# Kernel tuning notes

Hardware: AMD Instinct MI355X
Metric: run time of the kernel (lower is better)

Reference implementation:

```python
import jax, jax.numpy as jnp
import numpy as np

B, T, D, H, C = 128, 256, 256, 1024, 1000

def _xavier(k, shape):
    std = (2.0 / (shape[0] + shape[1])) ** 0.5
    return jax.random.normal(k, shape, dtype=jnp.float32) * std

def setup_inputs() -> dict:
    key = jax.random.key(0)
    ks = jax.random.split(key, 10)
    inp = {"x": jax.random.normal(ks[0], (B, T, D), dtype=jnp.float32)}
    for n, k in zip(["W_gx", "W_ix", "W_fx", "W_ox"], ks[1:5]):
        inp[n] = _xavier(k, (D, H))
    for n, k in zip(["W_gh", "W_ih", "W_fh", "W_oh"], ks[5:9]):
        inp[n] = _xavier(k, (H, H))
    inp["W_ph"] = _xavier(ks[9], (H, C))
    for n in ["b_g", "b_i", "b_f", "b_o"]:
        inp[n] = jnp.zeros((H,), dtype=jnp.float32)
    inp["b_p"] = jnp.zeros((C,), dtype=jnp.float32)
    return inp

def reference(x, W_gx, W_ix, W_fx, W_ox, W_gh, W_ih, W_fh, W_oh, W_ph,
              b_g, b_i, b_f, b_o, b_p):
    b, t, d = x.shape
    h_dim = W_gh.shape[0]
    # Precompute all input projections in batched GEMMs: [T, B, H]
    xg = jnp.einsum('btd,dh->tbh', x, W_gx) + b_g
    xi = jnp.einsum('btd,dh->tbh', x, W_ix) + b_i
    xf = jnp.einsum('btd,dh->tbh', x, W_fx) + b_f
    xo = jnp.einsum('btd,dh->tbh', x, W_ox) + b_o

    def step(carry, xs):
        h, c = carry
        pg, pi, pf, po = xs
        g = jnp.tanh(pg + h @ W_gh)
        i = jax.nn.sigmoid(pi + h @ W_ih)
        f = jax.nn.sigmoid(pf + h @ W_fh)
        o = jax.nn.sigmoid(po + h @ W_oh)
        c = g * i + c * f
        h = jnp.tanh(c) * o
        return (h, c), None

    h0 = jnp.zeros((b, h_dim), dtype=x.dtype)
    c0 = jnp.zeros((b, h_dim), dtype=x.dtype)
    (h_T, _), _ = jax.lax.scan(step, (h0, c0), (xg, xi, xf, xo))
    p = h_T @ W_ph + b_p  # [B, num_classes]
    return jax.nn.log_softmax(p, axis=1)
```

## Files before the change

### kernel.cpp

```cpp
#include <hip/hip_runtime.h>
#include <hip/hip_bf16.h>

#define B_ 128
#define T_ 256
#define D_ 256
#define H_ 1024
#define C_ 1000

typedef __attribute__((ext_vector_type(8))) short short8;
typedef __attribute__((ext_vector_type(4))) float floatx4;

static __device__ __forceinline__ unsigned short f2bf(float f) {
  unsigned int u = __builtin_bit_cast(unsigned int, f);
  u += 0x7fffu + ((u >> 16) & 1u);
  return (unsigned short)(u >> 16);
}
static __device__ __forceinline__ float bf2f(unsigned short s) {
  unsigned int u = ((unsigned int)s) << 16;
  return __builtin_bit_cast(float, u);
}
static __device__ __forceinline__ float sigm(float z) {
  return 1.0f / (1.0f + __expf(-z));
}
static __device__ __forceinline__ float tanh_fast(float z) {
  z = fminf(fmaxf(z, -15.f), 15.f);
  float e = __expf(2.f * z);
  return (e - 1.f) / (e + 1.f);
}

__global__ __launch_bounds__(256) void pack_all(
    const float* __restrict__ Wgx, const float* __restrict__ Wix,
    const float* __restrict__ Wfx, const float* __restrict__ Wox,
    const float* __restrict__ Wgh, const float* __restrict__ Wih,
    const float* __restrict__ Wfh, const float* __restrict__ Woh,
    unsigned short* __restrict__ Wp,
    const float* __restrict__ x, unsigned short* __restrict__ xb) {
  int blk = blockIdx.x;
  if (blk < 2560) {
    int t = blk * 256 + threadIdx.x;
    int L = t & 63;
    int g = (t >> 6) & 3;
    int rest = t >> 8;
    int kc = rest % 40;
    int jb = rest / 40;
    int n = L & 15, q = L >> 4;
    int j = jb * 16 + n;
    const float* Wh = (g == 0) ? Wgh : (g == 1) ? Wih : (g == 2) ? Wfh : Woh;
    const float* Wx = (g == 0) ? Wgx : (g == 1) ? Wix : (g == 2) ? Wfx : Wox;
    int k0 = kc * 32 + q * 8;
    unsigned int w[4];
#pragma unroll
    for (int i = 0; i < 4; i++) {
      int ka = k0 + 2 * i, kb = k0 + 2 * i + 1;
      float fa = (ka < H_) ? Wh[(size_t)ka * H_ + j] : Wx[(size_t)(ka - H_) * H_ + j];
      float fb = (kb < H_) ? Wh[(size_t)kb * H_ + j] : Wx[(size_t)(kb - H_) * H_ + j];
      w[i] = (unsigned int)f2bf(fa) | ((unsigned int)f2bf(fb) << 16);
    }
    uint4 v = {w[0], w[1], w[2], w[3]};
    *((uint4*)(Wp + (size_t)t * 8)) = v;
  } else {
    int idx = (blk - 2560) * 256 + threadIdx.x;
    int d8 = idx & 31;
    int tt = (idx >> 5) & 255;
    int b = idx >> 13;
    const float* src = x + ((size_t)b * T_ + tt) * D_ + d8 * 8;
    int rt = b >> 4, kcx = d8 >> 2, q = d8 & 3, m = b & 15;
    size_t dst = ((((size_t)tt * 8 + rt) * 8 + kcx) * 64 + (q * 16 + m)) * 8;
    unsigned int w[4];
#pragma unroll
    for (int i = 0; i < 4; i++) {
      float fa = src[2 * i], fb = src[2 * i + 1];
      w[i] = (unsigned int)f2bf(fa) | ((unsigned int)f2bf(fb) << 16);
    }
    uint4 v = {w[0], w[1], w[2], w[3]};
    *((uint4*)(xb + dst)) = v;
  }
}

__global__ __launch_bounds__(256, 1) void lstm_all(
    unsigned short* __restrict__ hb0, unsigned short* __restrict__ hb1,
    const unsigned short* __restrict__ Wp, const unsigned short* __restrict__ xb,
    const float* __restrict__ bg, const float* __restrict__ bi,
    const float* __restrict__ bf_, const float* __restrict__ bo,
    unsigned int* __restrict__ fl) {
  __shared__ unsigned short WL[32 * 4 * 64 * 8];
  __shared__ float xg[2][4][32][17];
  __shared__ float bb[4][16];

  const int tid = threadIdx.x;
  const int bid = blockIdx.x;
  const int jb = bid >> 2, rtq = bid & 3;
  const int w = tid >> 6, lane = tid & 63;
  const int rt01 = w & 1, kh = w >> 1;
  const int rt = rtq * 2 + rt01;
  const int grp = rtq * 64;

  {
    const uint4* src = (const uint4*)(Wp + (size_t)jb * (40 * 4 * 64 * 8));
    uint4* dst = (uint4*)WL;
#pragma unroll
    for (int i = 0; i < 32; i++) dst[i * 256 + tid] = src[i * 256 + tid];
  }
  if (tid < 64) {
    int g = tid >> 4, n = tid & 15;
    const float* bs = (g == 0) ? bg : (g == 1) ? bi : (g == 2) ? bf_ : bo;
    bb[g][n] = bs[jb * 16 + n];
  }
  {
    int rr = tid >> 3, n0 = (tid & 7) * 2;
    int r = rtq * 32 + rr;
    int rt_r = r >> 4, m = r & 15;
    int j = jb * 16 + n0;
    size_t dst = ((size_t)(rt_r * 32 + (j >> 5)) * 64 + (((j >> 3) & 3) * 16 + m)) * 8 + (j & 7);
    __hip_atomic_store((unsigned int*)(hb0 + dst), 0u, __ATOMIC_RELAXED,
                       __HIP_MEMORY_SCOPE_AGENT);
  }
  float c0 = 0.f, c1 = 0.f;

  const short8* BpX = (const short8*)Wp + (size_t)jb * (40 * 4 * 64) + lane;
  const short8* BL = (const short8*)WL + (size_t)kh * 4096 + lane;
  const int kc0 = kh * 16;
  const int kx0 = kh * 4;

  short8 bxw[4][4];
#pragma unroll
  for (int i = 0; i < 4; i++)
#pragma unroll
    for (int g = 0; g < 4; g++)
      bxw[i][g] = BpX[(size_t)((32 + kx0 + i) * 4 + g) * 64];

  __syncthreads();

  if (tid == 0)
    __hip_atomic_store(&fl[grp + jb], 1u, __ATOMIC_RELAXED, __HIP_MEMORY_SCOPE_AGENT);

  floatx4 xa0 = {0.f, 0.f, 0.f, 0.f};
  floatx4 xa1 = xa0, xa2 = xa0, xa3 = xa0;
  {
    const short8* Ax = (const short8*)xb + (((size_t)0 * 8 + rt) * 8 + kx0) * 64 + lane;
    short8 ax[4];
#pragma unroll
    for (int i = 0; i < 4; i++) ax[i] = Ax[(size_t)i * 64];
#pragma unroll
    for (int i = 0; i < 4; i++) {
      xa0 = __builtin_amdgcn_mfma_f32_16x16x32_bf16(ax[i], bxw[i][0], xa0, 0, 0, 0);
      xa1 = __builtin_amdgcn_mfma_f32_16x16x32_bf16(ax[i], bxw[i][1], xa1, 0, 0, 0);
      xa2 = __builtin_amdgcn_mfma_f32_16x16x32_bf16(ax[i], bxw[i][2], xa2, 0, 0, 0);
      xa3 = __builtin_amdgcn_mfma_f32_16x16x32_bf16(ax[i], bxw[i][3], xa3, 0, 0, 0);
    }
  }

  if (w == 0) {
    while (true) {
      unsigned int v = __hip_atomic_load(&fl[grp + lane], __ATOMIC_RELAXED,
                                         __HIP_MEMORY_SCOPE_AGENT);
      if (__all((int)(v >= 1u))) break;
    }
  }
  __syncthreads();
  asm volatile("" ::: "memory");

#pragma unroll 1
  for (int t = 0; t < 256; t++) {
    const unsigned short* hc = (t & 1) ? hb1 : hb0;
    unsigned short* hn = (t & 1) ? hb0 : hb1;

    const unsigned short* Ahp = hc + ((size_t)(rt * 32 + kc0) * 64 + lane) * 8;
    unsigned long long hq[32];
#pragma unroll
    for (int i = 0; i < 16; i++) {
      hq[2 * i] = __hip_atomic_load((const unsigned long long*)(Ahp + (size_t)i * 512),
                                    __ATOMIC_RELAXED, __HIP_MEMORY_SCOPE_AGENT);
      hq[2 * i + 1] = __hip_atomic_load((const unsigned long long*)(Ahp + (size_t)i * 512 + 4),
                                        __ATOMIC_RELAXED, __HIP_MEMORY_SCOPE_AGENT);
    }
    int tn = (t < 255) ? t + 1 : 255;
    const short8* Axn = (const short8*)xb + (((size_t)tn * 8 + rt) * 8 + kx0) * 64 + lane;
    short8 ax[4];
#pragma unroll
    for (int i = 0; i < 4; i++) ax[i] = Axn[(size_t)i * 64];

    floatx4 a0 = xa0, a1 = xa1, a2 = xa2, a3 = xa3;
#pragma unroll
    for (int kc = 0; kc < 16; kc++) {
      union { unsigned long long q[2]; short8 v; } u;
      u.q[0] = hq[2 * kc];
      u.q[1] = hq[2 * kc + 1];
      short8 av = u.v;
      short8 b0 = BL[(size_t)(kc * 4 + 0) * 64];
      short8 b1v = BL[(size_t)(kc * 4 + 1) * 64];
      short8 b2 = BL[(size_t)(kc * 4 + 2) * 64];
      short8 b3 = BL[(size_t)(kc * 4 + 3) * 64];
      a0 = __builtin_amdgcn_mfma_f32_16x16x32_bf16(av, b0, a0, 0, 0, 0);
      a1 = __builtin_amdgcn_mfma_f32_16x16x32_bf16(av, b1v, a1, 0, 0, 0);
      a2 = __builtin_amdgcn_mfma_f32_16x16x32_bf16(av, b2, a2, 0, 0, 0);
      a3 = __builtin_amdgcn_mfma_f32_16x16x32_bf16(av, b3, a3, 0, 0, 0);
    }

    {
      int cl = lane & 15, q = lane >> 4;
#pragma unroll
      for (int p = 0; p < 4; p++) {
        int rrow = rt01 * 16 + q * 4 + p;
        xg[kh][0][rrow][cl] = a0[p];
        xg[kh][1][rrow][cl] = a1[p];
        xg[kh][2][rrow][cl] = a2[p];
        xg[kh][3][rrow][cl] = a3[p];
      }
    }
    __syncthreads();

    {
      int rr = tid >> 3, n0 = (tid & 7) * 2;
      int r = rtq * 32 + rr;
      int rt_r = r >> 4, m = r & 15;
      unsigned int packed = 0;
#pragma unroll
      for (int u = 0; u < 2; u++) {
        int n = n0 + u;
        float pg = xg[0][0][rr][n] + xg[1][0][rr][n] + bb[0][n];
        float pi_ = xg[0][1][rr][n] + xg[1][1][rr][n] + bb[1][n];
        float pf = xg[0][2][rr][n] + xg[1][2][rr][n] + bb[2][n];
        float po = xg[0][3][rr][n] + xg[1][3][rr][n] + bb[3][n];
        float gg = tanh_fast(pg);
        float ii = sigm(pi_);
        float ff = sigm(pf);
        float oo = sigm(po);
        float cold = u ? c1 : c0;
        float cn = gg * ii + cold * ff;
        if (u) c1 = cn; else c0 = cn;
        float hv = tanh_fast(cn) * oo;
        packed |= ((unsigned int)f2bf(hv)) << (16 * u);
      }
      int j = jb * 16 + n0;
      size_t dst = ((size_t)(rt_r * 32 + (j >> 5)) * 64 + (((j >> 3) & 3) * 16 + m)) * 8 + (j & 7);
      __hip_atomic_store((unsigned int*)(hn + dst), packed, __ATOMIC_RELAXED,
                         __HIP_MEMORY_SCOPE_AGENT);
    }
    __syncthreads();

    if (tid == 0)
      __hip_atomic_store(&fl[grp + jb], (unsigned int)t + 2u, __ATOMIC_RELAXED,
                         __HIP_MEMORY_SCOPE_AGENT);

    xa0 = (floatx4){0.f, 0.f, 0.f, 0.f};
    xa1 = xa0; xa2 = xa0; xa3 = xa0;
#pragma unroll
    for (int i = 0; i < 4; i++) {
      xa0 = __builtin_amdgcn_mfma_f32_16x16x32_bf16(ax[i], bxw[i][0], xa0, 0, 0, 0);
      xa1 = __builtin_amdgcn_mfma_f32_16x16x32_bf16(ax[i], bxw[i][1], xa1, 0, 0, 0);
      xa2 = __builtin_amdgcn_mfma_f32_16x16x32_bf16(ax[i], bxw[i][2], xa2, 0, 0, 0);
      xa3 = __builtin_amdgcn_mfma_f32_16x16x32_bf16(ax[i], bxw[i][3], xa3, 0, 0, 0);
    }

    if (w == 0) {
      unsigned int tgt = (unsigned int)t + 2u;
      while (true) {
        unsigned int v = __hip_atomic_load(&fl[grp + lane], __ATOMIC_RELAXED,
                                           __HIP_MEMORY_SCOPE_AGENT);
        if (__all((int)(v >= tgt))) break;
      }
    }
    __syncthreads();
    asm volatile("" ::: "memory");
  }
}

__global__ __launch_bounds__(256) void proj_mfma(const unsigned short* __restrict__ hB,
                                                 const float* __restrict__ Wph,
                                                 const float* __restrict__ bp,
                                                 float* __restrict__ Lbuf) {
  __shared__ float pacc[4][16][17];
  const int tid = threadIdx.x;
  const int rt = blockIdx.x & 7;
  const int cb = blockIdx.x >> 3;
  const int w = tid >> 6, lane = tid & 63;
  const int n = lane & 15, q = lane >> 4;
  const int j = cb * 16 + n;
  const bool jv = (j < C_);

  floatx4 acc = {0.f, 0.f, 0.f, 0.f};
  const short8* Ah = (const short8*)hB + ((size_t)rt * 32) * 64 + lane;
#pragma unroll
  for (int kq = 0; kq < 8; kq++) {
    int kc = w * 8 + kq;
    short8 a = Ah[(size_t)kc * 64];
    int k0 = kc * 32 + q * 8;
    unsigned int wb[4];
#pragma unroll
    for (int i = 0; i < 4; i++) {
      float fa = jv ? Wph[(size_t)(k0 + 2 * i) * C_ + j] : 0.f;
      float fb = jv ? Wph[(size_t)(k0 + 2 * i + 1) * C_ + j] : 0.f;
      wb[i] = (unsigned int)f2bf(fa) | ((unsigned int)f2bf(fb) << 16);
    }
    union { unsigned int u[4]; short8 v; } bu;
    bu.u[0] = wb[0]; bu.u[1] = wb[1]; bu.u[2] = wb[2]; bu.u[3] = wb[3];
    acc = __builtin_amdgcn_mfma_f32_16x16x32_bf16(a, bu.v, acc, 0, 0, 0);
  }
#pragma unroll
  for (int p = 0; p < 4; p++) pacc[w][q * 4 + p][n] = acc[p];
  __syncthreads();

  {
    int r = tid >> 4, nn = tid & 15;
    int jj = cb * 16 + nn;
    float s = pacc[0][r][nn] + pacc[1][r][nn] + pacc[2][r][nn] + pacc[3][r][nn];
    s += (jj < C_) ? bp[jj] : 0.f;
    Lbuf[(size_t)(rt * 16 + r) * 1008 + jj] = s;
  }
}

__global__ __launch_bounds__(256) void softmax_k(const float* __restrict__ Lbuf,
                                                 float* __restrict__ out) {
  __shared__ float red[256];
  int row = blockIdx.x, tid = threadIdx.x;
  const float* Lr = Lbuf + (size_t)row * 1008;
  bool v3 = (tid + 768 < C_);
  float a0 = Lr[tid];
  float a1 = Lr[tid + 256];
  float a2 = Lr[tid + 512];
  float a3 = v3 ? Lr[tid + 768] : 0.f;

  float mx = fmaxf(fmaxf(a0, a1), a2);
  if (v3) mx = fmaxf(mx, a3);
  red[tid] = mx;
  __syncthreads();
  for (int s = 128; s > 0; s >>= 1) {
    if (tid < s) red[tid] = fmaxf(red[tid], red[tid + s]);
    __syncthreads();
  }
  float M = red[0];
  __syncthreads();
  float se = __expf(a0 - M) + __expf(a1 - M) + __expf(a2 - M);
  if (v3) se += __expf(a3 - M);
  red[tid] = se;
  __syncthreads();
  for (int s = 128; s > 0; s >>= 1) {
    if (tid < s) red[tid] += red[tid + s];
    __syncthreads();
  }
  float lse = M + logf(red[0]);
  out[(size_t)row * C_ + tid] = a0 - lse;
  out[(size_t)row * C_ + tid + 256] = a1 - lse;
  out[(size_t)row * C_ + tid + 512] = a2 - lse;
  if (v3) out[(size_t)row * C_ + tid + 768] = a3 - lse;
}

extern "C" void kernel_launch(void* const* d_in, const int* in_sizes, int n_in,
                              void* d_out, int out_size, void* d_ws, size_t ws_size,
                              hipStream_t stream) {
  const float* x   = (const float*)d_in[0];
  const float* Wgx = (const float*)d_in[1];
  const float* Wix = (const float*)d_in[2];
  const float* Wfx = (const float*)d_in[3];
  const float* Wox = (const float*)d_in[4];
  const float* Wgh = (const float*)d_in[5];
  const float* Wih = (const float*)d_in[6];
  const float* Wfh = (const float*)d_in[7];
  const float* Woh = (const float*)d_in[8];
  const float* Wph = (const float*)d_in[9];
  const float* bg  = (const float*)d_in[10];
  const float* bi  = (const float*)d_in[11];
  const float* bf  = (const float*)d_in[12];
  const float* bo  = (const float*)d_in[13];
  const float* bp  = (const float*)d_in[14];

  char* ws = (char*)d_ws;
  unsigned short* Wp = (unsigned short*)ws;
  size_t off = 10485760;
  unsigned short* xb = (unsigned short*)(ws + off);
  float* Lbuf = (float*)xb;
  off += 16777216;
  unsigned short* h0 = (unsigned short*)(ws + off); off += 262144;
  unsigned short* h1 = (unsigned short*)(ws + off); off += 262144;
  unsigned int* fl = (unsigned int*)(ws + off); off += 4096;

  hipMemsetAsync(fl, 0, 4096, stream);

  pack_all<<<6656, 256, 0, stream>>>(Wgx, Wix, Wfx, Wox, Wgh, Wih, Wfh, Woh, Wp, x, xb);

  void* args[] = {(void*)&h0, (void*)&h1, (void*)&Wp, (void*)&xb,
                  (void*)&bg, (void*)&bi, (void*)&bf, (void*)&bo, (void*)&fl};
  hipError_t cerr = hipLaunchCooperativeKernel((void*)lstm_all, dim3(256), dim3(256),
                                               args, 0, stream);
  if (cerr != hipSuccess) {
    lstm_all<<<256, 256, 0, stream>>>(h0, h1, Wp, xb, bg, bi, bf, bo, fl);
  }

  proj_mfma<<<504, 256, 0, stream>>>(h0, Wph, bp, Lbuf);
  softmax_k<<<128, 256, 0, stream>>>(Lbuf, (float*)d_out);
}
```

Baseline: 1.122 ms.

## Use per-step h ring buffer, split weights between registers and LDS, per-wave polling

Replaces the double-buffered hidden state with a ring of 257 buffers, one per timestep, when the workspace is large enough. Each step then reads a fresh address with plain vector loads instead of agent-scope atomic loads. Half of the recurrent weight tiles (gates g,i) now stay in registers and only gates f,o stay in LDS. Every wave polls the flags for its own half of the group instead of wave 0 polling followed by a block barrier, and the last step skips the final sync. The risks are much higher register pressure, a large workspace footprint, and a reliance on caches not serving stale lines at new addresses.

```diff
diff --git a/kernel.cpp b/kernel.cpp
--- a/kernel.cpp
+++ b/kernel.cpp
@@ -82,8 +82,8 @@
     const unsigned short* __restrict__ Wp, const unsigned short* __restrict__ xb,
     const float* __restrict__ bg, const float* __restrict__ bi,
     const float* __restrict__ bf_, const float* __restrict__ bo,
-    unsigned int* __restrict__ fl) {
-  __shared__ unsigned short WL[32 * 4 * 64 * 8];
+    unsigned int* __restrict__ fl, int ring) {
+  __shared__ unsigned short WL[32 * 2 * 64 * 8];
   __shared__ float xg[2][4][32][17];
   __shared__ float bb[4][16];
 
@@ -95,11 +95,17 @@
   const int rt = rtq * 2 + rt01;
   const int grp = rtq * 64;
 
+  (void)__hip_atomic_load(&fl[0], __ATOMIC_ACQUIRE, __HIP_MEMORY_SCOPE_AGENT);
+
   {
-    const uint4* src = (const uint4*)(Wp + (size_t)jb * (40 * 4 * 64 * 8));
-    uint4* dst = (uint4*)WL;
-#pragma unroll
-    for (int i = 0; i < 32; i++) dst[i * 256 + tid] = src[i * 256 + tid];
+    const uint4* srcW = (const uint4*)Wp + (size_t)jb * (40 * 4 * 64);
+    uint4* dstW = (uint4*)WL;
+#pragma unroll
+    for (int it = 0; it < 16; it++) {
+      int d = it * 256 + tid;
+      int kc = d >> 7, r = d & 127;
+      dstW[d] = srcW[(size_t)kc * 256 + 128 + r];
+    }
   }
   if (tid < 64) {
     int g = tid >> 4, n = tid & 15;
@@ -117,17 +123,24 @@
   }
   float c0 = 0.f, c1 = 0.f;
 
-  const short8* BpX = (const short8*)Wp + (size_t)jb * (40 * 4 * 64) + lane;
-  const short8* BL = (const short8*)WL + (size_t)kh * 4096 + lane;
+  const short8* BpH = (const short8*)Wp + (size_t)jb * (40 * 4 * 64) + lane;
+  const short8* BL2 = (const short8*)WL + (size_t)(kh * 32) * 64 + lane;
   const int kc0 = kh * 16;
   const int kx0 = kh * 4;
 
+  short8 bh0[16], bh1[16];
+#pragma unroll
+  for (int i = 0; i < 16; i++) {
+    int kc = kc0 + i;
+    bh0[i] = BpH[(size_t)(kc * 4 + 0) * 64];
+    bh1[i] = BpH[(size_t)(kc * 4 + 1) * 64];
+  }
   short8 bxw[4][4];
 #pragma unroll
   for (int i = 0; i < 4; i++)
 #pragma unroll
     for (int g = 0; g < 4; g++)
-      bxw[i][g] = BpX[(size_t)((32 + kx0 + i) * 4 + g) * 64];
+      bxw[i][g] = BpH[(size_t)((32 + kx0 + i) * 4 + g) * 64];
 
   __syncthreads();
 
@@ -137,7 +150,7 @@
   floatx4 xa0 = {0.f, 0.f, 0.f, 0.f};
   floatx4 xa1 = xa0, xa2 = xa0, xa3 = xa0;
   {
-    const short8* Ax = (const short8*)xb + (((size_t)0 * 8 + rt) * 8 + kx0) * 64 + lane;
+    const short8* Ax = (const short8*)xb + ((size_t)rt * 8 + kx0) * 64 + lane;
     short8 ax[4];
 #pragma unroll
     for (int i = 0; i < 4; i++) ax[i] = Ax[(size_t)i * 64];
@@ -149,50 +162,56 @@
       xa3 = __builtin_amdgcn_mfma_f32_16x16x32_bf16(ax[i], bxw[i][3], xa3, 0, 0, 0);
     }
   }
-
-  if (w == 0) {
+  {
     while (true) {
-      unsigned int v = __hip_atomic_load(&fl[grp + lane], __ATOMIC_RELAXED,
-                                         __HIP_MEMORY_SCOPE_AGENT);
+      unsigned int v = __hip_atomic_load(&fl[grp + kh * 32 + (lane & 31)],
+                                         __ATOMIC_RELAXED, __HIP_MEMORY_SCOPE_AGENT);
       if (__all((int)(v >= 1u))) break;
     }
   }
-  __syncthreads();
   asm volatile("" ::: "memory");
 
 #pragma unroll 1
   for (int t = 0; t < 256; t++) {
-    const unsigned short* hc = (t & 1) ? hb1 : hb0;
-    unsigned short* hn = (t & 1) ? hb0 : hb1;
-
-    const unsigned short* Ahp = hc + ((size_t)(rt * 32 + kc0) * 64 + lane) * 8;
-    unsigned long long hq[32];
-#pragma unroll
-    for (int i = 0; i < 16; i++) {
-      hq[2 * i] = __hip_atomic_load((const unsigned long long*)(Ahp + (size_t)i * 512),
-                                    __ATOMIC_RELAXED, __HIP_MEMORY_SCOPE_AGENT);
-      hq[2 * i + 1] = __hip_atomic_load((const unsigned long long*)(Ahp + (size_t)i * 512 + 4),
-                                        __ATOMIC_RELAXED, __HIP_MEMORY_SCOPE_AGENT);
-    }
-    int tn = (t < 255) ? t + 1 : 255;
-    const short8* Axn = (const short8*)xb + (((size_t)tn * 8 + rt) * 8 + kx0) * 64 + lane;
-    short8 ax[4];
-#pragma unroll
-    for (int i = 0; i < 4; i++) ax[i] = Axn[(size_t)i * 64];
+    const unsigned short* hc;
+    unsigned short* hn;
+    if (ring) {
+      hc = hb0 + (size_t)t * 131072;
+      hn = hb0 + (size_t)(t + 1) * 131072;
+    } else {
+      hc = (t & 1) ? hb1 : hb0;
+      hn = (t & 1) ? hb0 : hb1;
+    }
+
+    short8 hq[16];
+    if (ring) {
+      const short8* Ahp = (const short8*)hc + (size_t)(rt * 32 + kc0) * 64 + lane;
+#pragma unroll
+      for (int i = 0; i < 16; i++) hq[i] = Ahp[(size_t)i * 64];
+    } else {
+      const unsigned short* Ahp = hc + ((size_t)(rt * 32 + kc0) * 64 + lane) * 8;
+#pragma unroll
+      for (int i = 0; i < 16; i++) {
+        unsigned long long q0 = __hip_atomic_load(
+            (const unsigned long long*)(Ahp + (size_t)i * 512),
+            __ATOMIC_RELAXED, __HIP_MEMORY_SCOPE_AGENT);
+        unsigned long long q1 = __hip_atomic_load(
+            (const unsigned long long*)(Ahp + (size_t)i * 512 + 4),
+            __ATOMIC_RELAXED, __HIP_MEMORY_SCOPE_AGENT);
+        union { unsigned long long q[2]; short8 v; } u;
+        u.q[0] = q0; u.q[1] = q1;
+        hq[i] = u.v;
+      }
+    }
 
     floatx4 a0 = xa0, a1 = xa1, a2 = xa2, a3 = xa3;
 #pragma unroll
     for (int kc = 0; kc < 16; kc++) {
-      union { unsigned long long q[2]; short8 v; } u;
-      u.q[0] = hq[2 * kc];
-      u.q[1] = hq[2 * kc + 1];
-      short8 av = u.v;
-      short8 b0 = BL[(size_t)(kc * 4 + 0) * 64];
-      short8 b1v = BL[(size_t)(kc * 4 + 1) * 64];
-      short8 b2 = BL[(size_t)(kc * 4 + 2) * 64];
-      short8 b3 = BL[(size_t)(kc * 4 + 3) * 64];
-      a0 = __builtin_amdgcn_mfma_f32_16x16x32_bf16(av, b0, a0, 0, 0, 0);
-      a1 = __builtin_amdgcn_mfma_f32_16x16x32_bf16(av, b1v, a1, 0, 0, 0);
+      short8 av = hq[kc];
+      short8 b2 = BL2[(size_t)(kc * 2 + 0) * 64];
+      short8 b3 = BL2[(size_t)(kc * 2 + 1) * 64];
+      a0 = __builtin_amdgcn_mfma_f32_16x16x32_bf16(av, bh0[kc], a0, 0, 0, 0);
+      a1 = __builtin_amdgcn_mfma_f32_16x16x32_bf16(av, bh1[kc], a1, 0, 0, 0);
       a2 = __builtin_amdgcn_mfma_f32_16x16x32_bf16(av, b2, a2, 0, 0, 0);
       a3 = __builtin_amdgcn_mfma_f32_16x16x32_bf16(av, b3, a3, 0, 0, 0);
     }
@@ -208,6 +227,12 @@
         xg[kh][3][rrow][cl] = a3[p];
       }
     }
+    int tn = (t < 255) ? t + 1 : 255;
+    const short8* Axn = (const short8*)xb + (((size_t)tn * 8 + rt) * 8 + kx0) * 64 + lane;
+    short8 ax[4];
+#pragma unroll
+    for (int i = 0; i < 4; i++) ax[i] = Axn[(size_t)i * 64];
+
     __syncthreads();
 
     {
@@ -239,30 +264,31 @@
     }
     __syncthreads();
 
-    if (tid == 0)
-      __hip_atomic_store(&fl[grp + jb], (unsigned int)t + 2u, __ATOMIC_RELAXED,
-                         __HIP_MEMORY_SCOPE_AGENT);
-
-    xa0 = (floatx4){0.f, 0.f, 0.f, 0.f};
-    xa1 = xa0; xa2 = xa0; xa3 = xa0;
-#pragma unroll
-    for (int i = 0; i < 4; i++) {
-      xa0 = __builtin_amdgcn_mfma_f32_16x16x32_bf16(ax[i], bxw[i][0], xa0, 0, 0, 0);
-      xa1 = __builtin_amdgcn_mfma_f32_16x16x32_bf16(ax[i], bxw[i][1], xa1, 0, 0, 0);
-      xa2 = __builtin_amdgcn_mfma_f32_16x16x32_bf16(ax[i], bxw[i][2], xa2, 0, 0, 0);
-      xa3 = __builtin_amdgcn_mfma_f32_16x16x32_bf16(ax[i], bxw[i][3], xa3, 0, 0, 0);
-    }
-
-    if (w == 0) {
-      unsigned int tgt = (unsigned int)t + 2u;
-      while (true) {
-        unsigned int v = __hip_atomic_load(&fl[grp + lane], __ATOMIC_RELAXED,
-                                           __HIP_MEMORY_SCOPE_AGENT);
-        if (__all((int)(v >= tgt))) break;
+    if (t < 255) {
+      if (tid == 0)
+        __hip_atomic_store(&fl[grp + jb], (unsigned int)t + 2u, __ATOMIC_RELAXED,
+                           __HIP_MEMORY_SCOPE_AGENT);
+
+      xa0 = (floatx4){0.f, 0.f, 0.f, 0.f};
+      xa1 = xa0; xa2 = xa0; xa3 = xa0;
+#pragma unroll
+      for (int i = 0; i < 4; i++) {
+        xa0 = __builtin_amdgcn_mfma_f32_16x16x32_bf16(ax[i], bxw[i][0], xa0, 0, 0, 0);
+        xa1 = __builtin_amdgcn_mfma_f32_16x16x32_bf16(ax[i], bxw[i][1], xa1, 0, 0, 0);
+        xa2 = __builtin_amdgcn_mfma_f32_16x16x32_bf16(ax[i], bxw[i][2], xa2, 0, 0, 0);
+        xa3 = __builtin_amdgcn_mfma_f32_16x16x32_bf16(ax[i], bxw[i][3], xa3, 0, 0, 0);
       }
-    }
-    __syncthreads();
-    asm volatile("" ::: "memory");
+
+      {
+        unsigned int tgt = (unsigned int)t + 2u;
+        while (true) {
+          unsigned int v = __hip_atomic_load(&fl[grp + kh * 32 + (lane & 31)],
+                                             __ATOMIC_RELAXED, __HIP_MEMORY_SCOPE_AGENT);
+          if (__all((int)(v >= tgt))) break;
+        }
+      }
+      asm volatile("" ::: "memory");
+    }
   }
 }
 
@@ -371,22 +397,39 @@
   unsigned short* xb = (unsigned short*)(ws + off);
   float* Lbuf = (float*)xb;
   off += 16777216;
-  unsigned short* h0 = (unsigned short*)(ws + off); off += 262144;
-  unsigned short* h1 = (unsigned short*)(ws + off); off += 262144;
-  unsigned int* fl = (unsigned int*)(ws + off); off += 4096;
+
+  const size_t ring_need = off + 257ull * 262144ull + 4096ull;
+  int ring = (ws_size >= ring_need) ? 1 : 0;
+
+  unsigned short* hb0;
+  unsigned short* hb1;
+  unsigned short* hfin;
+  unsigned int* fl;
+  if (ring) {
+    hb0 = (unsigned short*)(ws + off); off += 257ull * 262144ull;
+    hb1 = hb0;
+    hfin = hb0 + 256ull * 131072ull;
+    fl = (unsigned int*)(ws + off); off += 4096;
+  } else {
+    hb0 = (unsigned short*)(ws + off); off += 262144;
+    hb1 = (unsigned short*)(ws + off); off += 262144;
+    hfin = hb0;
+    fl = (unsigned int*)(ws + off); off += 4096;
+  }
 
   hipMemsetAsync(fl, 0, 4096, stream);
 
   pack_all<<<6656, 256, 0, stream>>>(Wgx, Wix, Wfx, Wox, Wgh, Wih, Wfh, Woh, Wp, x, xb);
 
-  void* args[] = {(void*)&h0, (void*)&h1, (void*)&Wp, (void*)&xb,
-                  (void*)&bg, (void*)&bi, (void*)&bf, (void*)&bo, (void*)&fl};
+  void* args[] = {(void*)&hb0, (void*)&hb1, (void*)&Wp, (void*)&xb,
+                  (void*)&bg, (void*)&bi, (void*)&bf, (void*)&bo, (void*)&fl,
+                  (void*)&ring};
   hipError_t cerr = hipLaunchCooperativeKernel((void*)lstm_all, dim3(256), dim3(256),
                                                args, 0, stream);
   if (cerr != hipSuccess) {
-    lstm_all<<<256, 256, 0, stream>>>(h0, h1, Wp, xb, bg, bi, bf, bo, fl);
-  }
-
-  proj_mfma<<<504, 256, 0, stream>>>(h0, Wph, bp, Lbuf);
+    lstm_all<<<256, 256, 0, stream>>>(hb0, hb1, Wp, xb, bg, bi, bf, bo, fl, ring);
+  }
+
+  proj_mfma<<<504, 256, 0, stream>>>(hfin, Wph, bp, Lbuf);
   softmax_k<<<128, 256, 0, stream>>>(Lbuf, (float*)d_out);
 }
```

Result: slower. 1.983 ms (+76.7%).

## Switch LSTM recurrence to 32x32x16 MFMA with split-K LDS atomic reduction

Applied to the files above, without the earlier changes.

Moves the recurrent GEMM from 16x16x32 to 32x32x16 bf16 MFMA tiles. Each wave now covers all 32 rows for two gate pairs over a quarter of K, and the partial sums are combined through LDS float atomicAdds into an xg buffer that is pre-seeded with the biases. Weight, x and h packing layouts change to match the new MFMA operand format, and the projection kernel's h indexing is updated. Each wave now spins on the flags itself, which removes one barrier per step, but the LDS atomics and the extra barriers add contention.

```diff
diff --git a/kernel.cpp b/kernel.cpp
--- a/kernel.cpp
+++ b/kernel.cpp
@@ -9,6 +9,7 @@
 
 typedef __attribute__((ext_vector_type(8))) short short8;
 typedef __attribute__((ext_vector_type(4))) float floatx4;
+typedef __attribute__((ext_vector_type(16))) float floatx16;
 
 static __device__ __forceinline__ unsigned short f2bf(float f) {
   unsigned int u = __builtin_bit_cast(unsigned int, f);
@@ -39,15 +40,16 @@
   if (blk < 2560) {
     int t = blk * 256 + threadIdx.x;
     int L = t & 63;
-    int g = (t >> 6) & 3;
-    int rest = t >> 8;
-    int kc = rest % 40;
-    int jb = rest / 40;
-    int n = L & 15, q = L >> 4;
-    int j = jb * 16 + n;
+    int pair = (t >> 6) & 1;
+    int rest = t >> 7;
+    int kc16 = rest % 80;
+    int jb = rest / 80;
+    int col = L & 31;
+    int g = pair * 2 + (col >= 16 ? 1 : 0);
+    int j = jb * 16 + (col & 15);
     const float* Wh = (g == 0) ? Wgh : (g == 1) ? Wih : (g == 2) ? Wfh : Woh;
     const float* Wx = (g == 0) ? Wgx : (g == 1) ? Wix : (g == 2) ? Wfx : Wox;
-    int k0 = kc * 32 + q * 8;
+    int k0 = kc16 * 16 + (L >> 5) * 8;
     unsigned int w[4];
 #pragma unroll
     for (int i = 0; i < 4; i++) {
@@ -64,8 +66,8 @@
     int tt = (idx >> 5) & 255;
     int b = idx >> 13;
     const float* src = x + ((size_t)b * T_ + tt) * D_ + d8 * 8;
-    int rt = b >> 4, kcx = d8 >> 2, q = d8 & 3, m = b & 15;
-    size_t dst = ((((size_t)tt * 8 + rt) * 8 + kcx) * 64 + (q * 16 + m)) * 8;
+    int rt32 = b >> 5, kc16x = d8 >> 1, lane = (d8 & 1) * 32 + (b & 31);
+    size_t dst = ((((size_t)tt * 4 + rt32) * 16 + kc16x) * 64 + lane) * 8;
     unsigned int w[4];
 #pragma unroll
     for (int i = 0; i < 4; i++) {
@@ -83,186 +85,160 @@
     const float* __restrict__ bg, const float* __restrict__ bi,
     const float* __restrict__ bf_, const float* __restrict__ bo,
     unsigned int* __restrict__ fl) {
-  __shared__ unsigned short WL[32 * 4 * 64 * 8];
-  __shared__ float xg[2][4][32][17];
-  __shared__ float bb[4][16];
+  __shared__ unsigned short WL[65536];
+  __shared__ float xg[2][32][33];
 
   const int tid = threadIdx.x;
   const int bid = blockIdx.x;
   const int jb = bid >> 2, rtq = bid & 3;
-  const int w = tid >> 6, lane = tid & 63;
-  const int rt01 = w & 1, kh = w >> 1;
-  const int rt = rtq * 2 + rt01;
+  const int kq = tid >> 6, lane = tid & 63;
   const int grp = rtq * 64;
 
+  (void)__hip_atomic_load(&fl[0], __ATOMIC_ACQUIRE, __HIP_MEMORY_SCOPE_AGENT);
+
   {
-    const uint4* src = (const uint4*)(Wp + (size_t)jb * (40 * 4 * 64 * 8));
+    const uint4* src = (const uint4*)(Wp + (size_t)jb * 81920);
     uint4* dst = (uint4*)WL;
 #pragma unroll
     for (int i = 0; i < 32; i++) dst[i * 256 + tid] = src[i * 256 + tid];
   }
-  if (tid < 64) {
-    int g = tid >> 4, n = tid & 15;
-    const float* bs = (g == 0) ? bg : (g == 1) ? bi : (g == 2) ? bf_ : bo;
-    bb[g][n] = bs[jb * 16 + n];
-  }
-  {
-    int rr = tid >> 3, n0 = (tid & 7) * 2;
-    int r = rtq * 32 + rr;
-    int rt_r = r >> 4, m = r & 15;
-    int j = jb * 16 + n0;
-    size_t dst = ((size_t)(rt_r * 32 + (j >> 5)) * 64 + (((j >> 3) & 3) * 16 + m)) * 8 + (j & 7);
-    __hip_atomic_store((unsigned int*)(hb0 + dst), 0u, __ATOMIC_RELAXED,
-                       __HIP_MEMORY_SCOPE_AGENT);
-  }
+
+  const int rr = tid >> 3, n0 = (tid & 7) * 2;
+  const int j0 = jb * 16 + n0;
+  const float vbg0 = bg[j0], vbg1 = bg[j0 + 1];
+  const float vbi0 = bi[j0], vbi1 = bi[j0 + 1];
+  const float vbf0 = bf_[j0], vbf1 = bf_[j0 + 1];
+  const float vbo0 = bo[j0], vbo1 = bo[j0 + 1];
+  xg[0][rr][n0] = vbg0;      xg[0][rr][n0 + 1] = vbg1;
+  xg[0][rr][16 + n0] = vbi0; xg[0][rr][17 + n0] = vbi1;
+  xg[1][rr][n0] = vbf0;      xg[1][rr][n0 + 1] = vbf1;
+  xg[1][rr][16 + n0] = vbo0; xg[1][rr][17 + n0] = vbo1;
+
+  const size_t hz = ((size_t)(rtq * 64 + jb) * 64 + (n0 >> 3) * 32 + rr) * 8 + (n0 & 7);
+  __hip_atomic_store((unsigned int*)(hb0 + hz), 0u, __ATOMIC_RELAXED,
+                     __HIP_MEMORY_SCOPE_AGENT);
   float c0 = 0.f, c1 = 0.f;
 
-  const short8* BpX = (const short8*)Wp + (size_t)jb * (40 * 4 * 64) + lane;
-  const short8* BL = (const short8*)WL + (size_t)kh * 4096 + lane;
-  const int kc0 = kh * 16;
-  const int kx0 = kh * 4;
-
-  short8 bxw[4][4];
-#pragma unroll
-  for (int i = 0; i < 4; i++)
-#pragma unroll
-    for (int g = 0; g < 4; g++)
-      bxw[i][g] = BpX[(size_t)((32 + kx0 + i) * 4 + g) * 64];
+  const short8* BpX = (const short8*)Wp + (size_t)jb * 10240 + lane;
+  const short8* BL = (const short8*)WL + lane;
+  short8 bxw[4][2];
+#pragma unroll
+  for (int xi = 0; xi < 4; xi++) {
+    bxw[xi][0] = BpX[(size_t)((64 + kq * 4 + xi) * 2 + 0) * 64];
+    bxw[xi][1] = BpX[(size_t)((64 + kq * 4 + xi) * 2 + 1) * 64];
+  }
 
   __syncthreads();
 
   if (tid == 0)
     __hip_atomic_store(&fl[grp + jb], 1u, __ATOMIC_RELAXED, __HIP_MEMORY_SCOPE_AGENT);
 
-  floatx4 xa0 = {0.f, 0.f, 0.f, 0.f};
-  floatx4 xa1 = xa0, xa2 = xa0, xa3 = xa0;
+  const floatx16 vzero{};
+  floatx16 xa0 = vzero, xa1 = vzero;
   {
-    const short8* Ax = (const short8*)xb + (((size_t)0 * 8 + rt) * 8 + kx0) * 64 + lane;
-    short8 ax[4];
-#pragma unroll
-    for (int i = 0; i < 4; i++) ax[i] = Ax[(size_t)i * 64];
-#pragma unroll
-    for (int i = 0; i < 4; i++) {
-      xa0 = __builtin_amdgcn_mfma_f32_16x16x32_bf16(ax[i], bxw[i][0], xa0, 0, 0, 0);
-      xa1 = __builtin_amdgcn_mfma_f32_16x16x32_bf16(ax[i], bxw[i][1], xa1, 0, 0, 0);
-      xa2 = __builtin_amdgcn_mfma_f32_16x16x32_bf16(ax[i], bxw[i][2], xa2, 0, 0, 0);
-      xa3 = __builtin_amdgcn_mfma_f32_16x16x32_bf16(ax[i], bxw[i][3], xa3, 0, 0, 0);
-    }
-  }
-
-  if (w == 0) {
+    const short8* Axp = (const short8*)xb + ((size_t)rtq * 16 + kq * 4) * 64 + lane;
+#pragma unroll
+    for (int xi = 0; xi < 4; xi++) {
+      short8 ax = Axp[(size_t)xi * 64];
+      xa0 = __builtin_amdgcn_mfma_f32_32x32x16_bf16(ax, bxw[xi][0], xa0, 0, 0, 0);
+      xa1 = __builtin_amdgcn_mfma_f32_32x32x16_bf16(ax, bxw[xi][1], xa1, 0, 0, 0);
+    }
+  }
+  {
     while (true) {
-      unsigned int v = __hip_atomic_load(&fl[grp + lane], __ATOMIC_RELAXED,
-                                         __HIP_MEMORY_SCOPE_AGENT);
+      unsigned int v = __hip_atomic_load(&fl[grp + kq * 16 + (lane & 15)],
+                                         __ATOMIC_RELAXED, __HIP_MEMORY_SCOPE_AGENT);
       if (__all((int)(v >= 1u))) break;
     }
   }
-  __syncthreads();
   asm volatile("" ::: "memory");
+
+  const int hi5 = lane >> 5, colc = lane & 31;
 
 #pragma unroll 1
   for (int t = 0; t < 256; t++) {
     const unsigned short* hc = (t & 1) ? hb1 : hb0;
     unsigned short* hn = (t & 1) ? hb0 : hb1;
 
-    const unsigned short* Ahp = hc + ((size_t)(rt * 32 + kc0) * 64 + lane) * 8;
-    unsigned long long hq[32];
+    const unsigned short* Ahp = hc + ((size_t)(rtq * 64 + kq * 16) * 64 + lane) * 8;
+    short8 hq[16];
 #pragma unroll
     for (int i = 0; i < 16; i++) {
-      hq[2 * i] = __hip_atomic_load((const unsigned long long*)(Ahp + (size_t)i * 512),
-                                    __ATOMIC_RELAXED, __HIP_MEMORY_SCOPE_AGENT);
-      hq[2 * i + 1] = __hip_atomic_load((const unsigned long long*)(Ahp + (size_t)i * 512 + 4),
-                                        __ATOMIC_RELAXED, __HIP_MEMORY_SCOPE_AGENT);
-    }
+      union { unsigned long long q[2]; short8 v; } u;
+      u.q[0] = __hip_atomic_load((const unsigned long long*)(Ahp + (size_t)i * 512),
+                                 __ATOMIC_RELAXED, __HIP_MEMORY_SCOPE_AGENT);
+      u.q[1] = __hip_atomic_load((const unsigned long long*)(Ahp + (size_t)i * 512 + 4),
+                                 __ATOMIC_RELAXED, __HIP_MEMORY_SCOPE_AGENT);
+      hq[i] = u.v;
+    }
+
+#pragma unroll
+    for (int kc = 0; kc < 16; kc++) {
+      short8 b0 = BL[(size_t)((kq * 16 + kc) * 2 + 0) * 64];
+      short8 b1 = BL[(size_t)((kq * 16 + kc) * 2 + 1) * 64];
+      xa0 = __builtin_amdgcn_mfma_f32_32x32x16_bf16(hq[kc], b0, xa0, 0, 0, 0);
+      xa1 = __builtin_amdgcn_mfma_f32_32x32x16_bf16(hq[kc], b1, xa1, 0, 0, 0);
+    }
+
+#pragma unroll
+    for (int r = 0; r < 16; r++) {
+      int row = (r & 3) + 8 * (r >> 2) + 4 * hi5;
+      atomicAdd(&xg[0][row][colc], xa0[r]);
+      atomicAdd(&xg[1][row][colc], xa1[r]);
+    }
+
     int tn = (t < 255) ? t + 1 : 255;
-    const short8* Axn = (const short8*)xb + (((size_t)tn * 8 + rt) * 8 + kx0) * 64 + lane;
-    short8 ax[4];
-#pragma unroll
-    for (int i = 0; i < 4; i++) ax[i] = Axn[(size_t)i * 64];
-
-    floatx4 a0 = xa0, a1 = xa1, a2 = xa2, a3 = xa3;
-#pragma unroll
-    for (int kc = 0; kc < 16; kc++) {
-      union { unsigned long long q[2]; short8 v; } u;
-      u.q[0] = hq[2 * kc];
-      u.q[1] = hq[2 * kc + 1];
-      short8 av = u.v;
-      short8 b0 = BL[(size_t)(kc * 4 + 0) * 64];
-      short8 b1v = BL[(size_t)(kc * 4 + 1) * 64];
-      short8 b2 = BL[(size_t)(kc * 4 + 2) * 64];
-      short8 b3 = BL[(size_t)(kc * 4 + 3) * 64];
-      a0 = __builtin_amdgcn_mfma_f32_16x16x32_bf16(av, b0, a0, 0, 0, 0);
-      a1 = __builtin_amdgcn_mfma_f32_16x16x32_bf16(av, b1v, a1, 0, 0, 0);
-      a2 = __builtin_amdgcn_mfma_f32_16x16x32_bf16(av, b2, a2, 0, 0, 0);
-      a3 = __builtin_amdgcn_mfma_f32_16x16x32_bf16(av, b3, a3, 0, 0, 0);
-    }
+    const short8* Axp = (const short8*)xb + (((size_t)tn * 4 + rtq) * 16 + kq * 4) * 64 + lane;
+    short8 ax0 = Axp[0], ax1 = Axp[64], ax2 = Axp[128], ax3 = Axp[192];
+
+    __syncthreads();
 
     {
-      int cl = lane & 15, q = lane >> 4;
-#pragma unroll
-      for (int p = 0; p < 4; p++) {
-        int rrow = rt01 * 16 + q * 4 + p;
-        xg[kh][0][rrow][cl] = a0[p];
-        xg[kh][1][rrow][cl] = a1[p];
-        xg[kh][2][rrow][cl] = a2[p];
-        xg[kh][3][rrow][cl] = a3[p];
+      float pg0 = xg[0][rr][n0],      pg1 = xg[0][rr][n0 + 1];
+      float pi0 = xg[0][rr][16 + n0], pi1 = xg[0][rr][17 + n0];
+      float pf0 = xg[1][rr][n0],      pf1 = xg[1][rr][n0 + 1];
+      float po0 = xg[1][rr][16 + n0], po1 = xg[1][rr][17 + n0];
+      xg[0][rr][n0] = vbg0;      xg[0][rr][n0 + 1] = vbg1;
+      xg[0][rr][16 + n0] = vbi0; xg[0][rr][17 + n0] = vbi1;
+      xg[1][rr][n0] = vbf0;      xg[1][rr][n0 + 1] = vbf1;
+      xg[1][rr][16 + n0] = vbo0; xg[1][rr][17 + n0] = vbo1;
+
+      float cn0 = tanh_fast(pg0) * sigm(pi0) + c0 * sigm(pf0);
+      float cn1 = tanh_fast(pg1) * sigm(pi1) + c1 * sigm(pf1);
+      c0 = cn0; c1 = cn1;
+      float hv0 = tanh_fast(cn0) * sigm(po0);
+      float hv1 = tanh_fast(cn1) * sigm(po1);
+      unsigned int packed = (unsigned int)f2bf(hv0) | ((unsigned int)f2bf(hv1) << 16);
+      __hip_atomic_store((unsigned int*)(hn + hz), packed, __ATOMIC_RELAXED,
+                         __HIP_MEMORY_SCOPE_AGENT);
+    }
+    __syncthreads();
+
+    if (t < 255) {
+      if (tid == 0)
+        __hip_atomic_store(&fl[grp + jb], (unsigned int)t + 2u, __ATOMIC_RELAXED,
+                           __HIP_MEMORY_SCOPE_AGENT);
+
+      xa0 = vzero; xa1 = vzero;
+      xa0 = __builtin_amdgcn_mfma_f32_32x32x16_bf16(ax0, bxw[0][0], xa0, 0, 0, 0);
+      xa1 = __builtin_amdgcn_mfma_f32_32x32x16_bf16(ax0, bxw[0][1], xa1, 0, 0, 0);
+      xa0 = __builtin_amdgcn_mfma_f32_32x32x16_bf16(ax1, bxw[1][0], xa0, 0, 0, 0);
+      xa1 = __builtin_amdgcn_mfma_f32_32x32x16_bf16(ax1, bxw[1][1], xa1, 0, 0, 0);
+      xa0 = __builtin_amdgcn_mfma_f32_32x32x16_bf16(ax2, bxw[2][0], xa0, 0, 0, 0);
+      xa1 = __builtin_amdgcn_mfma_f32_32x32x16_bf16(ax2, bxw[2][1], xa1, 0, 0, 0);
+      xa0 = __builtin_amdgcn_mfma_f32_32x32x16_bf16(ax3, bxw[3][0], xa0, 0, 0, 0);
+      xa1 = __builtin_amdgcn_mfma_f32_32x32x16_bf16(ax3, bxw[3][1], xa1, 0, 0, 0);
+
+      {
+        unsigned int tgt = (unsigned int)t + 2u;
+        while (true) {
+          unsigned int v = __hip_atomic_load(&fl[grp + kq * 16 + (lane & 15)],
+                                             __ATOMIC_RELAXED, __HIP_MEMORY_SCOPE_AGENT);
+          if (__all((int)(v >= tgt))) break;
+        }
       }
-    }
-    __syncthreads();
-
-    {
-      int rr = tid >> 3, n0 = (tid & 7) * 2;
-      int r = rtq * 32 + rr;
-      int rt_r = r >> 4, m = r & 15;
-      unsigned int packed = 0;
-#pragma unroll
-      for (int u = 0; u < 2; u++) {
-        int n = n0 + u;
-        float pg = xg[0][0][rr][n] + xg[1][0][rr][n] + bb[0][n];
-        float pi_ = xg[0][1][rr][n] + xg[1][1][rr][n] + bb[1][n];
-        float pf = xg[0][2][rr][n] + xg[1][2][rr][n] + bb[2][n];
-        float po = xg[0][3][rr][n] + xg[1][3][rr][n] + bb[3][n];
-        float gg = tanh_fast(pg);
-        float ii = sigm(pi_);
-        float ff = sigm(pf);
-        float oo = sigm(po);
-        float cold = u ? c1 : c0;
-        float cn = gg * ii + cold * ff;
-        if (u) c1 = cn; else c0 = cn;
-        float hv = tanh_fast(cn) * oo;
-        packed |= ((unsigned int)f2bf(hv)) << (16 * u);
-      }
-      int j = jb * 16 + n0;
-      size_t dst = ((size_t)(rt_r * 32 + (j >> 5)) * 64 + (((j >> 3) & 3) * 16 + m)) * 8 + (j & 7);
-      __hip_atomic_store((unsigned int*)(hn + dst), packed, __ATOMIC_RELAXED,
-                         __HIP_MEMORY_SCOPE_AGENT);
-    }
-    __syncthreads();
-
-    if (tid == 0)
-      __hip_atomic_store(&fl[grp + jb], (unsigned int)t + 2u, __ATOMIC_RELAXED,
-                         __HIP_MEMORY_SCOPE_AGENT);
-
-    xa0 = (floatx4){0.f, 0.f, 0.f, 0.f};
-    xa1 = xa0; xa2 = xa0; xa3 = xa0;
-#pragma unroll
-    for (int i = 0; i < 4; i++) {
-      xa0 = __builtin_amdgcn_mfma_f32_16x16x32_bf16(ax[i], bxw[i][0], xa0, 0, 0, 0);
-      xa1 = __builtin_amdgcn_mfma_f32_16x16x32_bf16(ax[i], bxw[i][1], xa1, 0, 0, 0);
-      xa2 = __builtin_amdgcn_mfma_f32_16x16x32_bf16(ax[i], bxw[i][2], xa2, 0, 0, 0);
-      xa3 = __builtin_amdgcn_mfma_f32_16x16x32_bf16(ax[i], bxw[i][3], xa3, 0, 0, 0);
-    }
-
-    if (w == 0) {
-      unsigned int tgt = (unsigned int)t + 2u;
-      while (true) {
-        unsigned int v = __hip_atomic_load(&fl[grp + lane], __ATOMIC_RELAXED,
-                                           __HIP_MEMORY_SCOPE_AGENT);
-        if (__all((int)(v >= tgt))) break;
-      }
-    }
-    __syncthreads();
-    asm volatile("" ::: "memory");
+      asm volatile("" ::: "memory");
+    }
   }
 }
 
@@ -280,11 +256,12 @@
   const bool jv = (j < C_);
 
   floatx4 acc = {0.f, 0.f, 0.f, 0.f};
-  const short8* Ah = (const short8*)hB + ((size_t)rt * 32) * 64 + lane;
+  const short8* Ah = (const short8*)hB;
 #pragma unroll
   for (int kq = 0; kq < 8; kq++) {
     int kc = w * 8 + kq;
-    short8 a = Ah[(size_t)kc * 64];
+    short8 a = Ah[(((size_t)(rt >> 1) * 64) + kc * 2 + (q >> 1)) * 64 +
+                  (q & 1) * 32 + (rt & 1) * 16 + n];
     int k0 = kc * 32 + q * 8;
     unsigned int wb[4];
 #pragma unroll
@@ -371,22 +348,22 @@
   unsigned short* xb = (unsigned short*)(ws + off);
   float* Lbuf = (float*)xb;
   off += 16777216;
-  unsigned short* h0 = (unsigned short*)(ws + off); off += 262144;
-  unsigned short* h1 = (unsigned short*)(ws + off); off += 262144;
+  unsigned short* hb0 = (unsigned short*)(ws + off); off += 262144;
+  unsigned short* hb1 = (unsigned short*)(ws + off); off += 262144;
   unsigned int* fl = (unsigned int*)(ws + off); off += 4096;
 
   hipMemsetAsync(fl, 0, 4096, stream);
 
   pack_all<<<6656, 256, 0, stream>>>(Wgx, Wix, Wfx, Wox, Wgh, Wih, Wfh, Woh, Wp, x, xb);
 
-  void* args[] = {(void*)&h0, (void*)&h1, (void*)&Wp, (void*)&xb,
+  void* args[] = {(void*)&hb0, (void*)&hb1, (void*)&Wp, (void*)&xb,
                   (void*)&bg, (void*)&bi, (void*)&bf, (void*)&bo, (void*)&fl};
   hipError_t cerr = hipLaunchCooperativeKernel((void*)lstm_all, dim3(256), dim3(256),
                                                args, 0, stream);
   if (cerr != hipSuccess) {
-    lstm_all<<<256, 256, 0, stream>>>(h0, h1, Wp, xb, bg, bi, bf, bo, fl);
-  }
-
-  proj_mfma<<<504, 256, 0, stream>>>(h0, Wph, bp, Lbuf);
+    lstm_all<<<256, 256, 0, stream>>>(hb0, hb1, Wp, xb, bg, bi, bf, bo, fl);
+  }
+
+  proj_mfma<<<504, 256, 0, stream>>>(hb0, Wph, bp, Lbuf);
   softmax_k<<<128, 256, 0, stream>>>(Lbuf, (float*)d_out);
 }
```

New measurement: 3.807 ms. 239% more time.

## Move per-step flag wait into all waves and prefetch LDS weights before spin

Applied to the files above, without the earlier changes.

Each wave now spins on its own half of the group flags at the top of each step instead of wave 0 spinning and then a block-wide barrier, removing one __syncthreads per timestep. Half of the recurrent weight fragments are preloaded from LDS into registers before the wait, so the LDS latency overlaps with the spin. The next-step x loads are moved later, and the final step skips the flag publish and the x-projection. This raises register pressure and relies on subtler cross-wave ordering for correctness.

```diff
diff --git a/kernel.cpp b/kernel.cpp
--- a/kernel.cpp
+++ b/kernel.cpp
@@ -95,6 +95,8 @@
   const int rt = rtq * 2 + rt01;
   const int grp = rtq * 64;
 
+  (void)__hip_atomic_load(&fl[0], __ATOMIC_ACQUIRE, __HIP_MEMORY_SCOPE_AGENT);
+
   {
     const uint4* src = (const uint4*)(Wp + (size_t)jb * (40 * 4 * 64 * 8));
     uint4* dst = (uint4*)WL;
@@ -137,7 +139,7 @@
   floatx4 xa0 = {0.f, 0.f, 0.f, 0.f};
   floatx4 xa1 = xa0, xa2 = xa0, xa3 = xa0;
   {
-    const short8* Ax = (const short8*)xb + (((size_t)0 * 8 + rt) * 8 + kx0) * 64 + lane;
+    const short8* Ax = (const short8*)xb + ((size_t)rt * 8 + kx0) * 64 + lane;
     short8 ax[4];
 #pragma unroll
     for (int i = 0; i < 4; i++) ax[i] = Ax[(size_t)i * 64];
@@ -150,20 +152,27 @@
     }
   }
 
-  if (w == 0) {
-    while (true) {
-      unsigned int v = __hip_atomic_load(&fl[grp + lane], __ATOMIC_RELAXED,
-                                         __HIP_MEMORY_SCOPE_AGENT);
-      if (__all((int)(v >= 1u))) break;
-    }
-  }
-  __syncthreads();
-  asm volatile("" ::: "memory");
-
 #pragma unroll 1
   for (int t = 0; t < 256; t++) {
     const unsigned short* hc = (t & 1) ? hb1 : hb0;
     unsigned short* hn = (t & 1) ? hb0 : hb1;
+
+    short8 pb0[16], pb1[16];
+#pragma unroll
+    for (int i = 0; i < 16; i++) {
+      pb0[i] = BL[(size_t)(i * 4 + 0) * 64];
+      pb1[i] = BL[(size_t)(i * 4 + 1) * 64];
+    }
+
+    {
+      unsigned int tgt = (unsigned int)t + 1u;
+      while (true) {
+        unsigned int v = __hip_atomic_load(&fl[grp + kh * 32 + (lane & 31)],
+                                           __ATOMIC_RELAXED, __HIP_MEMORY_SCOPE_AGENT);
+        if (__all((int)(v >= tgt))) break;
+      }
+    }
+    asm volatile("" ::: "memory");
 
     const unsigned short* Ahp = hc + ((size_t)(rt * 32 + kc0) * 64 + lane) * 8;
     unsigned long long hq[32];
@@ -174,11 +183,6 @@
       hq[2 * i + 1] = __hip_atomic_load((const unsigned long long*)(Ahp + (size_t)i * 512 + 4),
                                         __ATOMIC_RELAXED, __HIP_MEMORY_SCOPE_AGENT);
     }
-    int tn = (t < 255) ? t + 1 : 255;
-    const short8* Axn = (const short8*)xb + (((size_t)tn * 8 + rt) * 8 + kx0) * 64 + lane;
-    short8 ax[4];
-#pragma unroll
-    for (int i = 0; i < 4; i++) ax[i] = Axn[(size_t)i * 64];
 
     floatx4 a0 = xa0, a1 = xa1, a2 = xa2, a3 = xa3;
 #pragma unroll
@@ -187,12 +191,10 @@
       u.q[0] = hq[2 * kc];
       u.q[1] = hq[2 * kc + 1];
       short8 av = u.v;
-      short8 b0 = BL[(size_t)(kc * 4 + 0) * 64];
-      short8 b1v = BL[(size_t)(kc * 4 + 1) * 64];
       short8 b2 = BL[(size_t)(kc * 4 + 2) * 64];
       short8 b3 = BL[(size_t)(kc * 4 + 3) * 64];
-      a0 = __builtin_amdgcn_mfma_f32_16x16x32_bf16(av, b0, a0, 0, 0, 0);
-      a1 = __builtin_amdgcn_mfma_f32_16x16x32_bf16(av, b1v, a1, 0, 0, 0);
+      a0 = __builtin_amdgcn_mfma_f32_16x16x32_bf16(av, pb0[kc], a0, 0, 0, 0);
+      a1 = __builtin_amdgcn_mfma_f32_16x16x32_bf16(av, pb1[kc], a1, 0, 0, 0);
       a2 = __builtin_amdgcn_mfma_f32_16x16x32_bf16(av, b2, a2, 0, 0, 0);
       a3 = __builtin_amdgcn_mfma_f32_16x16x32_bf16(av, b3, a3, 0, 0, 0);
     }
@@ -208,6 +210,12 @@
         xg[kh][3][rrow][cl] = a3[p];
       }
     }
+    int tn = (t < 255) ? t + 1 : 255;
+    const short8* Axn = (const short8*)xb + (((size_t)tn * 8 + rt) * 8 + kx0) * 64 + lane;
+    short8 ax[4];
+#pragma unroll
+    for (int i = 0; i < 4; i++) ax[i] = Axn[(size_t)i * 64];
+
     __syncthreads();
 
     {
@@ -239,30 +247,21 @@
     }
     __syncthreads();
 
-    if (tid == 0)
-      __hip_atomic_store(&fl[grp + jb], (unsigned int)t + 2u, __ATOMIC_RELAXED,
-                         __HIP_MEMORY_SCOPE_AGENT);
-
-    xa0 = (floatx4){0.f, 0.f, 0.f, 0.f};
-    xa1 = xa0; xa2 = xa0; xa3 = xa0;
-#pragma unroll
-    for (int i = 0; i < 4; i++) {
-      xa0 = __builtin_amdgcn_mfma_f32_16x16x32_bf16(ax[i], bxw[i][0], xa0, 0, 0, 0);
-      xa1 = __builtin_amdgcn_mfma_f32_16x16x32_bf16(ax[i], bxw[i][1], xa1, 0, 0, 0);
-      xa2 = __builtin_amdgcn_mfma_f32_16x16x32_bf16(ax[i], bxw[i][2], xa2, 0, 0, 0);
-      xa3 = __builtin_amdgcn_mfma_f32_16x16x32_bf16(ax[i], bxw[i][3], xa3, 0, 0, 0);
-    }
-
-    if (w == 0) {
-      unsigned int tgt = (unsigned int)t + 2u;
-      while (true) {
-        unsigned int v = __hip_atomic_load(&fl[grp + lane], __ATOMIC_RELAXED,
-                                           __HIP_MEMORY_SCOPE_AGENT);
-        if (__all((int)(v >= tgt))) break;
+    if (t < 255) {
+      if (tid == 0)
+        __hip_atomic_store(&fl[grp + jb], (unsigned int)t + 2u, __ATOMIC_RELAXED,
+                           __HIP_MEMORY_SCOPE_AGENT);
+
+      xa0 = (floatx4){0.f, 0.f, 0.f, 0.f};
+      xa1 = xa0; xa2 = xa0; xa3 = xa0;
+#pragma unroll
+      for (int i = 0; i < 4; i++) {
+        xa0 = __builtin_amdgcn_mfma_f32_16x16x32_bf16(ax[i], bxw[i][0], xa0, 0, 0, 0);
+        xa1 = __builtin_amdgcn_mfma_f32_16x16x32_bf16(ax[i], bxw[i][1], xa1, 0, 0, 0);
+        xa2 = __builtin_amdgcn_mfma_f32_16x16x32_bf16(ax[i], bxw[i][2], xa2, 0, 0, 0);
+        xa3 = __builtin_amdgcn_mfma_f32_16x16x32_bf16(ax[i], bxw[i][3], xa3, 0, 0, 0);
       }
     }
-    __syncthreads();
-    asm volatile("" ::: "memory");
   }
 }
 
@@ -371,22 +370,22 @@
   unsigned short* xb = (unsigned short*)(ws + off);
   float* Lbuf = (float*)xb;
   off += 16777216;
-  unsigned short* h0 = (unsigned short*)(ws + off); off += 262144;
-  unsigned short* h1 = (unsigned short*)(ws + off); off += 262144;
+  unsigned short* hb0 = (unsigned short*)(ws + off); off += 262144;
+  unsigned short* hb1 = (unsigned short*)(ws + off); off += 262144;
   unsigned int* fl = (unsigned int*)(ws + off); off += 4096;
 
   hipMemsetAsync(fl, 0, 4096, stream);
 
   pack_all<<<6656, 256, 0, stream>>>(Wgx, Wix, Wfx, Wox, Wgh, Wih, Wfh, Woh, Wp, x, xb);
 
-  void* args[] = {(void*)&h0, (void*)&h1, (void*)&Wp, (void*)&xb,
+  void* args[] = {(void*)&hb0, (void*)&hb1, (void*)&Wp, (void*)&xb,
                   (void*)&bg, (void*)&bi, (void*)&bf, (void*)&bo, (void*)&fl};
   hipError_t cerr = hipLaunchCooperativeKernel((void*)lstm_all, dim3(256), dim3(256),
                                                args, 0, stream);
   if (cerr != hipSuccess) {
-    lstm_all<<<256, 256, 0, stream>>>(h0, h1, Wp, xb, bg, bi, bf, bo, fl);
-  }
-
-  proj_mfma<<<504, 256, 0, stream>>>(h0, Wph, bp, Lbuf);
+    lstm_all<<<256, 256, 0, stream>>>(hb0, hb1, Wp, xb, bg, bi, bf, bo, fl);
+  }
+
+  proj_mfma<<<504, 256, 0, stream>>>(hb0, Wph, bp, Lbuf);
   softmax_k<<<128, 256, 0, stream>>>(Lbuf, (float*)d_out);
 }
```

After: 1.141 ms. Within noise of the previous version (+1.7%).
